# Kernel optimization log

Hardware: AMD Instinct MI355X
Metric: run time of the kernel (lower is better)

The kernel has to match this reference:

```python
import jax, jax.numpy as jnp
import numpy as np

B, S, D = 2, 2048, 512
E, H, TOP_K = 8, 1024, 2
SCALE = 1.0


def setup_inputs() -> dict:
    key = jax.random.key(0)
    ks = jax.random.split(key, 7)
    s = lambda fan_in: 1.0 / np.sqrt(fan_in)
    return {
        "x": jax.random.normal(ks[0], (B, S, D), dtype=jnp.float32),
        "gate_w": jax.random.normal(ks[1], (E, D), dtype=jnp.float32) * s(D),
        "w1": jax.random.normal(ks[2], (E, H, D), dtype=jnp.float32) * s(D),
        "w2": jax.random.normal(ks[3], (E, D, H), dtype=jnp.float32) * s(H),
        "sg_gate": jax.random.normal(ks[4], (H, D), dtype=jnp.float32) * s(D),
        "sg_up": jax.random.normal(ks[5], (H, D), dtype=jnp.float32) * s(D),
        "sg_down": jax.random.normal(ks[6], (D, H), dtype=jnp.float32) * s(H),
    }


def reference(x, gate_w, w1, w2, sg_gate, sg_up, sg_down):
    b, s_len, d = x.shape
    xf = x.reshape(-1, d)                      # [N, D]
    n = xf.shape[0]

    # --- TopKRouter: logits -> top-k -> softmax over the k selected logits ---
    logits = (xf @ gate_w.T) * SCALE           # [N, E]
    topk_w, idx = jax.lax.top_k(logits, TOP_K)  # [N, K]
    topk_w = jax.nn.softmax(topk_w, axis=-1)
    # per-token combine weights scattered to expert slots: [N, E]
    comb = jnp.zeros((n, E), dtype=xf.dtype).at[jnp.arange(n)[:, None], idx].add(topk_w)

    # --- Routed experts (dense masked compute; weight 0 for unrouted) ---
    h = jax.nn.silu(jnp.einsum('td,ehd->teh', xf, w1))   # [N, E, H]
    eo = jnp.einsum('teh,edh->ted', h, w2)               # [N, E, D]
    routed = jnp.einsum('te,ted->td', comb, eo)          # [N, D]

    # --- Shared expert (SwiGLU), n_shared_experts = 1 ---
    shared = (jax.nn.silu(xf @ sg_gate.T) * (xf @ sg_up.T)) @ sg_down.T

    return (routed + shared).reshape(b, s_len, d)
```

## Files before the change

### kernel.cpp

```cpp
#include <hip/hip_runtime.h>
#include <hip/hip_bf16.h>


#define NTOK 4096
#define DDIM 512
#define HDIM 1024
#define NEXP 8
#define CAP  4096

typedef unsigned short u16;
typedef __attribute__((ext_vector_type(8))) short short8;
typedef __attribute__((ext_vector_type(4))) float f32x4;

__device__ __forceinline__ u16 f2bf(float f) {
  unsigned u = __float_as_uint(f);
  u += 0x7fffu + ((u >> 16) & 1u);
  return (u16)(u >> 16);
}
__device__ __forceinline__ float bf2f(u16 v) {
  return __uint_as_float(((unsigned)v) << 16);
}
__device__ __forceinline__ float silu_f(float v) { return v / (1.0f + __expf(-v)); }

__device__ __forceinline__ void gload16(const u16* g, u16* l) {
  __builtin_amdgcn_global_load_lds((const __attribute__((address_space(1))) void*)g,
                                   (__attribute__((address_space(3))) void*)l, 16, 0, 0);
}

__global__ __launch_bounds__(256) void prep(
    const float* __restrict__ x,   const float* __restrict__ gw,
    const float* __restrict__ w1,
    const float* __restrict__ sgg, const float* __restrict__ sgu,
    u16* __restrict__ Xb, u16* __restrict__ W1b,
    u16* __restrict__ SGGb, u16* __restrict__ SGUb,
    int* __restrict__ tIdx, float2* __restrict__ tW) {
  if (blockIdx.x < NTOK / 4) {
    const int lane = threadIdx.x & 63;
    const int wid  = threadIdx.x >> 6;
    const int t = blockIdx.x * 4 + wid;
    const float4* xr = (const float4*)(x + (size_t)t * DDIM + lane * 8);
    const float4 x0 = xr[0], x1 = xr[1];
    short8 xbv;
    xbv[0]=f2bf(x0.x); xbv[1]=f2bf(x0.y); xbv[2]=f2bf(x0.z); xbv[3]=f2bf(x0.w);
    xbv[4]=f2bf(x1.x); xbv[5]=f2bf(x1.y); xbv[6]=f2bf(x1.z); xbv[7]=f2bf(x1.w);
    *(short8*)&Xb[(size_t)t * DDIM + lane * 8] = xbv;
    float p[NEXP];
#pragma unroll
    for (int e = 0; e < NEXP; ++e) {
      const float4* gr = (const float4*)(gw + (size_t)e * DDIM + lane * 8);
      const float4 g0 = gr[0], g1 = gr[1];
      p[e] = x0.x*g0.x + x0.y*g0.y + x0.z*g0.z + x0.w*g0.w +
             x1.x*g1.x + x1.y*g1.y + x1.z*g1.z + x1.w*g1.w;
    }
#pragma unroll
    for (int e = 0; e < NEXP; ++e) {
#pragma unroll
      for (int m = 32; m >= 1; m >>= 1) p[e] += __shfl_xor(p[e], m);
    }
    if (lane == 0) {
      int i0 = 0; float v0 = p[0];
#pragma unroll
      for (int e = 1; e < NEXP; ++e) if (p[e] > v0) { v0 = p[e]; i0 = e; }
      int i1 = -1; float v1 = -3.0e38f;
#pragma unroll
      for (int e = 0; e < NEXP; ++e) if (e != i0 && p[e] > v1) { v1 = p[e]; i1 = e; }
      const float ex1 = __expf(v1 - v0);
      const float inv = 1.0f / (1.0f + ex1);
      tIdx[t] = i0 | (i1 << 4);
      tW[t] = make_float2(inv, ex1 * inv);
    }
  } else {
    constexpr int NW1 = NEXP * HDIM * DDIM / 4;
    constexpr int NSG = HDIM * DDIM / 4;
    constexpr int TOT = NW1 + 2 * NSG;
    int i = (blockIdx.x - NTOK / 4) * 256 + threadIdx.x;
    const int stride = (gridDim.x - NTOK / 4) * 256;
    for (; i < TOT; i += stride) {
      const float* s; u16* d; int j = i;
      if (j < NW1)               { s = w1;  d = W1b;  }
      else if ((j -= NW1) < NSG) { s = sgg; d = SGGb; }
      else        { j -= NSG;      s = sgu; d = SGUb; }
      float4 v = ((const float4*)s)[j];
      ushort4 o;
      o.x = f2bf(v.x); o.y = f2bf(v.y); o.z = f2bf(v.z); o.w = f2bf(v.w);
      ((ushort4*)d)[j] = o;
    }
  }
}

__global__ __launch_bounds__(256) void build_lists(
    const int* __restrict__ tIdx,
    int* __restrict__ counts, int* __restrict__ elist) {
  const int e = blockIdx.x;
  __shared__ int cnt;
  if (threadIdx.x == 0) cnt = 0;
  __syncthreads();
  const int lane = threadIdx.x & 63;
  int* el = elist + e * CAP;
  for (int base = 0; base < NTOK; base += 256) {
    const int t = base + threadIdx.x;
    const int pk = tIdx[t];
#pragma unroll
    for (int slot = 0; slot < 2; ++slot) {
      const bool m = (((pk >> (slot * 4)) & 15) == e);
      const unsigned long long b = __ballot(m);
      const int my  = __popcll(b & ((1ull << lane) - 1));
      const int tot = __popcll(b);
      int wbase = 0;
      if (lane == 0 && tot) wbase = atomicAdd(&cnt, tot);
      wbase = __shfl(wbase, 0);
      if (m) el[wbase + my] = t * 2 + slot;
    }
  }
  __syncthreads();
  if (threadIdx.x == 0) counts[e] = cnt;
}

#define BUFE (128 * 32)

__global__ __launch_bounds__(512, 6) void gemm_up(
    const u16* __restrict__ Xb, const u16* __restrict__ W1b,
    const u16* __restrict__ SGGb, const u16* __restrict__ SGUb,
    const float* __restrict__ w2f, const float* __restrict__ sgdf,
    u16* __restrict__ W2b, u16* __restrict__ SGDb,
    u16* __restrict__ Hbuf, u16* __restrict__ ACT,
    const int* __restrict__ counts, const int* __restrict__ elist) {
  constexpr int KDIM = DDIM, KSTEP = KDIM / 32;
  const int z = blockIdx.z;

  if (z == 0) {
    constexpr int NW2 = NEXP * DDIM * HDIM / 4;
    constexpr int NSG = HDIM * DDIM / 4;
    constexpr int TOT = NW2 + NSG;
    const int cb = blockIdx.x + 16 * blockIdx.y;
    int i = cb * 512 + threadIdx.x;
    const int stride = 512 * 512;
    for (; i < TOT; i += stride) {
      const float* s; u16* d; int j = i;
      if (j < NW2) { s = w2f; d = W2b; }
      else         { j -= NW2; s = sgdf; d = SGDb; }
      float4 v = ((const float4*)s)[j];
      ushort4 o;
      o.x = f2bf(v.x); o.y = f2bf(v.y); o.z = f2bf(v.z); o.w = f2bf(v.w);
      ((ushort4*)d)[j] = o;
    }
    return;
  }

  const int m0 = blockIdx.y * 128;
  const bool routed = (z <= NEXP);

  int mlim; const u16* Bp = nullptr; const int* lst = nullptr;
  if (routed) {
    const int e = z - 1;
    if (blockIdx.x >= 8) return;
    mlim = counts[e];
    lst = elist + e * CAP;
    Bp = W1b + (size_t)e * HDIM * KDIM;
  } else {
    mlim = NTOK;
  }
  if (m0 >= mlim) return;

  __shared__ __align__(16) u16 As[3 * BUFE];
  __shared__ __align__(16) u16 Bs[3 * BUFE];
  __shared__ int rowE[128];

  const int tid = threadIdx.x;
  const int wid = tid >> 6, lane = tid & 63;

  if (routed) {
    if (tid < 128) {
      int idx = m0 + tid; if (idx > mlim - 1) idx = mlim - 1;
      rowE[tid] = lst[idx];
    }
    __syncthreads();
  }

  const int row = tid >> 2;
  const int kcp = ((tid & 3) - ((row >> 1) & 3)) & 3;
  const int arow = routed ? (rowE[row] >> 1) : (m0 + row);
  const u16* aG = Xb + (size_t)arow * KDIM + kcp * 8;
  const u16* bG;
  if (routed) {
    bG = Bp + (size_t)(blockIdx.x * 128 + row) * KDIM + kcp * 8;
  } else {
    const int n0 = blockIdx.x * 64;
    bG = (row < 64) ? SGGb + (size_t)(n0 + row) * KDIM + kcp * 8
                    : SGUb + (size_t)(n0 + row - 64) * KDIM + kcp * 8;
  }

  const int lr = lane & 15, lk = lane >> 4;
  const int rslot = ((lk + ((lr >> 1) & 3)) & 3) * 8;

  auto STAGE = [&](int kt, int c) {
    gload16(aG + kt * 32, As + c * BUFE + tid * 8);
    gload16(bG + kt * 32, Bs + c * BUFE + tid * 8);
  };

  const f32x4 zero = {0.f, 0.f, 0.f, 0.f};

  if (routed) {
    const int n0 = blockIdx.x * 128;
    const int wm = (wid >> 2) * 64, wn = (wid & 3) * 32;
    f32x4 acc[4][2];
#pragma unroll
    for (int i = 0; i < 4; ++i)
#pragma unroll
      for (int j = 0; j < 2; ++j) acc[i][j] = zero;

    STAGE(0, 0); STAGE(1, 1);
    for (int kt = 0; kt < KSTEP; ++kt) {
      if (kt + 1 < KSTEP) asm volatile("s_waitcnt vmcnt(2)" ::: "memory");
      else                asm volatile("s_waitcnt vmcnt(0)" ::: "memory");
      __builtin_amdgcn_s_barrier();
      __builtin_amdgcn_sched_barrier(0);
      if (kt + 2 < KSTEP) STAGE(kt + 2, (kt + 2) % 3);
      const u16* ab = As + (kt % 3) * BUFE;
      const u16* bb = Bs + (kt % 3) * BUFE;
      short8 a[4], b[2];
#pragma unroll
      for (int i = 0; i < 4; ++i)
        a[i] = *(const short8*)&ab[(wm + i * 16 + lr) * 32 + rslot];
#pragma unroll
      for (int j = 0; j < 2; ++j)
        b[j] = *(const short8*)&bb[(wn + j * 16 + lr) * 32 + rslot];
      __builtin_amdgcn_s_setprio(1);
#pragma unroll
      for (int i = 0; i < 4; ++i)
#pragma unroll
        for (int j = 0; j < 2; ++j)
          acc[i][j] = __builtin_amdgcn_mfma_f32_16x16x32_bf16(a[i], b[j], acc[i][j], 0, 0, 0);
      __builtin_amdgcn_s_setprio(0);
    }

#pragma unroll
    for (int i = 0; i < 4; ++i) {
#pragma unroll
      for (int j = 0; j < 2; ++j) {
        const int col = n0 + wn + j * 16 + lr;
#pragma unroll
        for (int r = 0; r < 4; ++r) {
          const int m = wm + i * 16 + lk * 4 + r;
          if (m0 + m < mlim)
            Hbuf[(size_t)rowE[m] * HDIM + col] = f2bf(silu_f(acc[i][j][r]));
        }
      }
    }
  } else {
    const int n0 = blockIdx.x * 64;
    const int wm = (wid >> 2) * 64, ws = (wid & 3) * 16;
    f32x4 ag[4], au[4];
#pragma unroll
    for (int i = 0; i < 4; ++i) { ag[i] = zero; au[i] = zero; }

    STAGE(0, 0); STAGE(1, 1);
    for (int kt = 0; kt < KSTEP; ++kt) {
      if (kt + 1 < KSTEP) asm volatile("s_waitcnt vmcnt(2)" ::: "memory");
      else                asm volatile("s_waitcnt vmcnt(0)" ::: "memory");
      __builtin_amdgcn_s_barrier();
      __builtin_amdgcn_sched_barrier(0);
      if (kt + 2 < KSTEP) STAGE(kt + 2, (kt + 2) % 3);
      const u16* ab = As + (kt % 3) * BUFE;
      const u16* bb = Bs + (kt % 3) * BUFE;
      short8 a[4], bg, bu;
#pragma unroll
      for (int i = 0; i < 4; ++i)
        a[i] = *(const short8*)&ab[(wm + i * 16 + lr) * 32 + rslot];
      bg = *(const short8*)&bb[(ws + lr) * 32 + rslot];
      bu = *(const short8*)&bb[(64 + ws + lr) * 32 + rslot];
      __builtin_amdgcn_s_setprio(1);
#pragma unroll
      for (int i = 0; i < 4; ++i) {
        ag[i] = __builtin_amdgcn_mfma_f32_16x16x32_bf16(a[i], bg, ag[i], 0, 0, 0);
        au[i] = __builtin_amdgcn_mfma_f32_16x16x32_bf16(a[i], bu, au[i], 0, 0, 0);
      }
      __builtin_amdgcn_s_setprio(0);
    }

#pragma unroll
    for (int i = 0; i < 4; ++i) {
      const int col = n0 + ws + lr;
#pragma unroll
      for (int r = 0; r < 4; ++r) {
        const int m = wm + i * 16 + lk * 4 + r;
        ACT[(size_t)(m0 + m) * HDIM + col] = f2bf(silu_f(ag[i][r]) * au[i][r]);
      }
    }
  }
}

__global__ __launch_bounds__(512, 6) void gemm_down(
    const u16* __restrict__ Hbuf, const u16* __restrict__ W2b,
    const u16* __restrict__ ACT,  const u16* __restrict__ SGDb,
    u16* __restrict__ eo0, u16* __restrict__ eo1,
    float* __restrict__ sh0, float* __restrict__ sh1,
    const int* __restrict__ counts, const int* __restrict__ elist) {
  constexpr int KFULL = HDIM;
  constexpr int KSTEP = 512 / 32;
  const int z = blockIdx.z;
  const int n0 = blockIdx.x * 128;
  const int m0 = blockIdx.y * 128;
  const bool routed = (z < 2 * NEXP);
  const int khalf = routed ? (z & 1) : (z - 2 * NEXP);
  const int koff = khalf * 512;

  int mlim; const u16* Ap; const u16* Bp; const int* lst = nullptr;
  if (routed) {
    const int e = z >> 1;
    mlim = counts[e];
    lst = elist + e * CAP;
    Ap = Hbuf;
    Bp = W2b + (size_t)e * DDIM * KFULL;
  } else {
    mlim = NTOK;
    Ap = ACT;
    Bp = SGDb;
  }
  if (m0 >= mlim) return;

  __shared__ __align__(16) u16 As[3 * BUFE];
  __shared__ __align__(16) u16 Bs[3 * BUFE];
  __shared__ int rowE[128];

  const int tid = threadIdx.x;
  const int wid = tid >> 6, lane = tid & 63;

  if (routed) {
    if (tid < 128) {
      int idx = m0 + tid; if (idx > mlim - 1) idx = mlim - 1;
      rowE[tid] = lst[idx];
    }
    __syncthreads();
  }

  const int row = tid >> 2;
  const int kcp = ((tid & 3) - ((row >> 1) & 3)) & 3;
  const int arow = routed ? rowE[row] : (m0 + row);
  const u16* aG = Ap + (size_t)arow * KFULL + koff + kcp * 8;
  const u16* bG = Bp + (size_t)(n0 + row) * KFULL + koff + kcp * 8;

  const int wm = (wid >> 2) * 64, wn = (wid & 3) * 32;
  const int lr = lane & 15, lk = lane >> 4;
  const int rslot = ((lk + ((lr >> 1) & 3)) & 3) * 8;

  const f32x4 zero = {0.f, 0.f, 0.f, 0.f};
  f32x4 acc[4][2];
#pragma unroll
  for (int i = 0; i < 4; ++i)
#pragma unroll
    for (int j = 0; j < 2; ++j) acc[i][j] = zero;

  auto STAGE = [&](int kt, int c) {
    gload16(aG + kt * 32, As + c * BUFE + tid * 8);
    gload16(bG + kt * 32, Bs + c * BUFE + tid * 8);
  };

  STAGE(0, 0); STAGE(1, 1);
  for (int kt = 0; kt < KSTEP; ++kt) {
    if (kt + 1 < KSTEP) asm volatile("s_waitcnt vmcnt(2)" ::: "memory");
    else                asm volatile("s_waitcnt vmcnt(0)" ::: "memory");
    __builtin_amdgcn_s_barrier();
    __builtin_amdgcn_sched_barrier(0);
    if (kt + 2 < KSTEP) STAGE(kt + 2, (kt + 2) % 3);
    const u16* ab = As + (kt % 3) * BUFE;
    const u16* bb = Bs + (kt % 3) * BUFE;
    short8 a[4], b[2];
#pragma unroll
    for (int i = 0; i < 4; ++i)
      a[i] = *(const short8*)&ab[(wm + i * 16 + lr) * 32 + rslot];
#pragma unroll
    for (int j = 0; j < 2; ++j)
      b[j] = *(const short8*)&bb[(wn + j * 16 + lr) * 32 + rslot];
    __builtin_amdgcn_s_setprio(1);
#pragma unroll
    for (int i = 0; i < 4; ++i)
#pragma unroll
      for (int j = 0; j < 2; ++j)
        acc[i][j] = __builtin_amdgcn_mfma_f32_16x16x32_bf16(a[i], b[j], acc[i][j], 0, 0, 0);
    __builtin_amdgcn_s_setprio(0);
  }

#pragma unroll
  for (int i = 0; i < 4; ++i) {
#pragma unroll
    for (int j = 0; j < 2; ++j) {
      const int col = n0 + wn + j * 16 + lr;
#pragma unroll
      for (int r = 0; r < 4; ++r) {
        const int m = wm + i * 16 + lk * 4 + r;
        if (routed) {
          if (m0 + m < mlim) {
            u16* dst = khalf ? eo1 : eo0;
            dst[(size_t)rowE[m] * DDIM + col] = f2bf(acc[i][j][r]);
          }
        } else {
          float* dst = khalf ? sh1 : sh0;
          dst[(size_t)(m0 + m) * DDIM + col] = acc[i][j][r];
        }
      }
    }
  }
}

__global__ __launch_bounds__(256) void combine_kernel(
    const u16* __restrict__ eo0, const u16* __restrict__ eo1,
    const float* __restrict__ sh0, const float* __restrict__ sh1,
    const float2* __restrict__ tW, float* __restrict__ out) {
  const int g = blockIdx.x * 256 + threadIdx.x;
  const int t = g >> 6;
  const int c0 = (g & 63) * 8;
  const float2 w = tW[t];
  const size_t r0 = (size_t)(t * 2) * DDIM + c0;
  const size_t r1 = (size_t)(t * 2 + 1) * DDIM + c0;
  const short8 a0 = *(const short8*)&eo0[r0];
  const short8 a1 = *(const short8*)&eo0[r1];
  const short8 b0 = *(const short8*)&eo1[r0];
  const short8 b1 = *(const short8*)&eo1[r1];
  const size_t so = (size_t)t * DDIM + c0;
  const float4 s0a = ((const float4*)(sh0 + so))[0];
  const float4 s0b = ((const float4*)(sh0 + so))[1];
  const float4 s1a = ((const float4*)(sh1 + so))[0];
  const float4 s1b = ((const float4*)(sh1 + so))[1];
  float o[8];
  o[0]=s0a.x+s1a.x; o[1]=s0a.y+s1a.y; o[2]=s0a.z+s1a.z; o[3]=s0a.w+s1a.w;
  o[4]=s0b.x+s1b.x; o[5]=s0b.y+s1b.y; o[6]=s0b.z+s1b.z; o[7]=s0b.w+s1b.w;
#pragma unroll
  for (int k = 0; k < 8; ++k)
    o[k] += w.x * (bf2f((u16)a0[k]) + bf2f((u16)b0[k])) +
            w.y * (bf2f((u16)a1[k]) + bf2f((u16)b1[k]));
  float4 v0 = {o[0], o[1], o[2], o[3]};
  float4 v1 = {o[4], o[5], o[6], o[7]};
  ((float4*)(out + so))[0] = v0;
  ((float4*)(out + so))[1] = v1;
}

extern "C" void kernel_launch(void* const* d_in, const int* in_sizes, int n_in,
                              void* d_out, int out_size, void* d_ws, size_t ws_size,
                              hipStream_t stream) {
  const float* x    = (const float*)d_in[0];
  const float* gw   = (const float*)d_in[1];
  const float* w1   = (const float*)d_in[2];
  const float* w2   = (const float*)d_in[3];
  const float* sgg  = (const float*)d_in[4];
  const float* sgu  = (const float*)d_in[5];
  const float* sgd  = (const float*)d_in[6];
  float* out = (float*)d_out;

  char* ws = (char*)d_ws;
  size_t off = 0;
  auto take = [&](size_t bytes) {
    size_t r = off; off += (bytes + 255) & ~(size_t)255; return r;
  };
  int*    counts = (int*)   (ws + take(NEXP * sizeof(int)));
  int*    elist  = (int*)   (ws + take((size_t)NEXP * CAP * sizeof(int)));
  int*    tIdx   = (int*)   (ws + take((size_t)NTOK * sizeof(int)));
  float2* tW     = (float2*)(ws + take((size_t)NTOK * sizeof(float2)));
  u16*    Xb     = (u16*)   (ws + take((size_t)NTOK * DDIM * 2));
  u16*    W1b    = (u16*)   (ws + take((size_t)NEXP * HDIM * DDIM * 2));
  u16*    W2b    = (u16*)   (ws + take((size_t)NEXP * DDIM * HDIM * 2));
  u16*    SGGb   = (u16*)   (ws + take((size_t)HDIM * DDIM * 2));
  u16*    SGUb   = (u16*)   (ws + take((size_t)HDIM * DDIM * 2));
  u16*    SGDb   = (u16*)   (ws + take((size_t)DDIM * HDIM * 2));
  u16*    Hbuf   = (u16*)   (ws + take((size_t)NTOK * 2 * HDIM * 2));
  u16*    ACT    = (u16*)   (ws + take((size_t)NTOK * HDIM * 2));
  u16*    eo0    = (u16*)   (ws + take((size_t)NTOK * 2 * DDIM * 2));
  u16*    eo1    = (u16*)   (ws + take((size_t)NTOK * 2 * DDIM * 2));
  float*  sh0    = (float*) (ws + take((size_t)NTOK * DDIM * 4));
  float*  sh1    = (float*) (ws + take((size_t)NTOK * DDIM * 4));
  if (off > ws_size) return;

  prep<<<dim3(3072), 256, 0, stream>>>(x, gw, w1, sgg, sgu,
                                       Xb, W1b, SGGb, SGUb, tIdx, tW);
  build_lists<<<NEXP, 256, 0, stream>>>(tIdx, counts, elist);
  gemm_up<<<dim3(16, 32, NEXP + 2), 512, 0, stream>>>(
      Xb, W1b, SGGb, SGUb, w2, sgd, W2b, SGDb, Hbuf, ACT, counts, elist);
  gemm_down<<<dim3(DDIM / 128, 32, 2 * NEXP + 2), 512, 0, stream>>>(
      Hbuf, W2b, ACT, SGDb, eo0, eo1, sh0, sh1, counts, elist);
  combine_kernel<<<NTOK * 64 / 256, 256, 0, stream>>>(eo0, eo1, sh0, sh1, tW, out);
}
```

Baseline: 105.0 us.

## Widen GEMM output tiles to 128x256 in up and down projections

Doubles the N dimension of each block tile in gemm_up and gemm_down (routed 128x256, shared 128 gate+128 up columns), so each wave computes a 64x64 sub-tile with 16 MFMA accumulators. The goal is more MFMA work per LDS load of the A operand and fewer blocks re-reading the same activation rows. The cost is more shared memory and registers per block, lowered to an occupancy target of 4, and half as many blocks in a grid that is already sparse for the routed experts.

```diff
diff --git a/kernel.cpp b/kernel.cpp
--- a/kernel.cpp
+++ b/kernel.cpp
@@ -116,9 +116,10 @@
   if (threadIdx.x == 0) counts[e] = cnt;
 }
 
-#define BUFE (128 * 32)
-
-__global__ __launch_bounds__(512, 6) void gemm_up(
+#define ABUF (128 * 32)
+#define BBUF (256 * 32)
+
+__global__ __launch_bounds__(512, 4) void gemm_up(
     const u16* __restrict__ Xb, const u16* __restrict__ W1b,
     const u16* __restrict__ SGGb, const u16* __restrict__ SGUb,
     const float* __restrict__ w2f, const float* __restrict__ sgdf,
@@ -132,9 +133,9 @@
     constexpr int NW2 = NEXP * DDIM * HDIM / 4;
     constexpr int NSG = HDIM * DDIM / 4;
     constexpr int TOT = NW2 + NSG;
-    const int cb = blockIdx.x + 16 * blockIdx.y;
+    const int cb = blockIdx.x + 8 * blockIdx.y;
     int i = cb * 512 + threadIdx.x;
-    const int stride = 512 * 512;
+    const int stride = 256 * 512;
     for (; i < TOT; i += stride) {
       const float* s; u16* d; int j = i;
       if (j < NW2) { s = w2f; d = W2b; }
@@ -152,8 +153,8 @@
 
   int mlim; const u16* Bp = nullptr; const int* lst = nullptr;
   if (routed) {
+    if (blockIdx.x >= 4) return;
     const int e = z - 1;
-    if (blockIdx.x >= 8) return;
     mlim = counts[e];
     lst = elist + e * CAP;
     Bp = W1b + (size_t)e * HDIM * KDIM;
@@ -162,8 +163,8 @@
   }
   if (m0 >= mlim) return;
 
-  __shared__ __align__(16) u16 As[3 * BUFE];
-  __shared__ __align__(16) u16 Bs[3 * BUFE];
+  __shared__ __align__(16) u16 As[3 * ABUF];
+  __shared__ __align__(16) u16 Bs[3 * BBUF];
   __shared__ int rowE[128];
 
   const int tid = threadIdx.x;
@@ -177,59 +178,65 @@
     __syncthreads();
   }
 
-  const int row = tid >> 2;
-  const int kcp = ((tid & 3) - ((row >> 1) & 3)) & 3;
-  const int arow = routed ? (rowE[row] >> 1) : (m0 + row);
-  const u16* aG = Xb + (size_t)arow * KDIM + kcp * 8;
-  const u16* bG;
+  const int rowA = tid >> 2;
+  const int rowB0 = rowA, rowB1 = 128 + rowA;
+  const int kcpA  = ((tid & 3) - ((rowA  >> 1) & 3)) & 3;
+  const int kcpB0 = ((tid & 3) - ((rowB0 >> 1) & 3)) & 3;
+  const int kcpB1 = ((tid & 3) - ((rowB1 >> 1) & 3)) & 3;
+  const int arow = routed ? (rowE[rowA] >> 1) : (m0 + rowA);
+  const u16* aG = Xb + (size_t)arow * KDIM + kcpA * 8;
+  const u16 *bG0, *bG1;
   if (routed) {
-    bG = Bp + (size_t)(blockIdx.x * 128 + row) * KDIM + kcp * 8;
+    const int n0 = blockIdx.x * 256;
+    bG0 = Bp + (size_t)(n0 + rowB0) * KDIM + kcpB0 * 8;
+    bG1 = Bp + (size_t)(n0 + rowB1) * KDIM + kcpB1 * 8;
   } else {
-    const int n0 = blockIdx.x * 64;
-    bG = (row < 64) ? SGGb + (size_t)(n0 + row) * KDIM + kcp * 8
-                    : SGUb + (size_t)(n0 + row - 64) * KDIM + kcp * 8;
+    const int n0 = blockIdx.x * 128;
+    bG0 = SGGb + (size_t)(n0 + rowB0) * KDIM + kcpB0 * 8;
+    bG1 = SGUb + (size_t)(n0 + rowB1 - 128) * KDIM + kcpB1 * 8;
   }
 
   const int lr = lane & 15, lk = lane >> 4;
   const int rslot = ((lk + ((lr >> 1) & 3)) & 3) * 8;
 
   auto STAGE = [&](int kt, int c) {
-    gload16(aG + kt * 32, As + c * BUFE + tid * 8);
-    gload16(bG + kt * 32, Bs + c * BUFE + tid * 8);
+    gload16(aG  + kt * 32, As + c * ABUF + tid * 8);
+    gload16(bG0 + kt * 32, Bs + c * BBUF + tid * 8);
+    gload16(bG1 + kt * 32, Bs + c * BBUF + (tid + 512) * 8);
   };
 
   const f32x4 zero = {0.f, 0.f, 0.f, 0.f};
 
   if (routed) {
-    const int n0 = blockIdx.x * 128;
-    const int wm = (wid >> 2) * 64, wn = (wid & 3) * 32;
-    f32x4 acc[4][2];
+    const int n0 = blockIdx.x * 256;
+    const int wm = (wid >> 2) * 64, wn = (wid & 3) * 64;
+    f32x4 acc[4][4];
 #pragma unroll
     for (int i = 0; i < 4; ++i)
 #pragma unroll
-      for (int j = 0; j < 2; ++j) acc[i][j] = zero;
+      for (int j = 0; j < 4; ++j) acc[i][j] = zero;
 
     STAGE(0, 0); STAGE(1, 1);
     for (int kt = 0; kt < KSTEP; ++kt) {
-      if (kt + 1 < KSTEP) asm volatile("s_waitcnt vmcnt(2)" ::: "memory");
+      if (kt + 1 < KSTEP) asm volatile("s_waitcnt vmcnt(3)" ::: "memory");
       else                asm volatile("s_waitcnt vmcnt(0)" ::: "memory");
       __builtin_amdgcn_s_barrier();
       __builtin_amdgcn_sched_barrier(0);
       if (kt + 2 < KSTEP) STAGE(kt + 2, (kt + 2) % 3);
-      const u16* ab = As + (kt % 3) * BUFE;
-      const u16* bb = Bs + (kt % 3) * BUFE;
-      short8 a[4], b[2];
+      const u16* ab = As + (kt % 3) * ABUF;
+      const u16* bb = Bs + (kt % 3) * BBUF;
+      short8 a[4], b[4];
 #pragma unroll
       for (int i = 0; i < 4; ++i)
         a[i] = *(const short8*)&ab[(wm + i * 16 + lr) * 32 + rslot];
 #pragma unroll
-      for (int j = 0; j < 2; ++j)
+      for (int j = 0; j < 4; ++j)
         b[j] = *(const short8*)&bb[(wn + j * 16 + lr) * 32 + rslot];
       __builtin_amdgcn_s_setprio(1);
 #pragma unroll
       for (int i = 0; i < 4; ++i)
 #pragma unroll
-        for (int j = 0; j < 2; ++j)
+        for (int j = 0; j < 4; ++j)
           acc[i][j] = __builtin_amdgcn_mfma_f32_16x16x32_bf16(a[i], b[j], acc[i][j], 0, 0, 0);
       __builtin_amdgcn_s_setprio(0);
     }
@@ -237,7 +244,7 @@
 #pragma unroll
     for (int i = 0; i < 4; ++i) {
 #pragma unroll
-      for (int j = 0; j < 2; ++j) {
+      for (int j = 0; j < 4; ++j) {
         const int col = n0 + wn + j * 16 + lr;
 #pragma unroll
         for (int r = 0; r < 4; ++r) {
@@ -248,49 +255,60 @@
       }
     }
   } else {
-    const int n0 = blockIdx.x * 64;
-    const int wm = (wid >> 2) * 64, ws = (wid & 3) * 16;
-    f32x4 ag[4], au[4];
-#pragma unroll
-    for (int i = 0; i < 4; ++i) { ag[i] = zero; au[i] = zero; }
+    const int n0 = blockIdx.x * 128;
+    const int wm = (wid >> 2) * 64, ws = (wid & 3) * 32;
+    f32x4 ag[4][2], au[4][2];
+#pragma unroll
+    for (int i = 0; i < 4; ++i)
+#pragma unroll
+      for (int j = 0; j < 2; ++j) { ag[i][j] = zero; au[i][j] = zero; }
 
     STAGE(0, 0); STAGE(1, 1);
     for (int kt = 0; kt < KSTEP; ++kt) {
-      if (kt + 1 < KSTEP) asm volatile("s_waitcnt vmcnt(2)" ::: "memory");
+      if (kt + 1 < KSTEP) asm volatile("s_waitcnt vmcnt(3)" ::: "memory");
       else                asm volatile("s_waitcnt vmcnt(0)" ::: "memory");
       __builtin_amdgcn_s_barrier();
       __builtin_amdgcn_sched_barrier(0);
       if (kt + 2 < KSTEP) STAGE(kt + 2, (kt + 2) % 3);
-      const u16* ab = As + (kt % 3) * BUFE;
-      const u16* bb = Bs + (kt % 3) * BUFE;
-      short8 a[4], bg, bu;
+      const u16* ab = As + (kt % 3) * ABUF;
+      const u16* bb = Bs + (kt % 3) * BBUF;
+      short8 a[4], bg[2], bu[2];
 #pragma unroll
       for (int i = 0; i < 4; ++i)
         a[i] = *(const short8*)&ab[(wm + i * 16 + lr) * 32 + rslot];
-      bg = *(const short8*)&bb[(ws + lr) * 32 + rslot];
-      bu = *(const short8*)&bb[(64 + ws + lr) * 32 + rslot];
+#pragma unroll
+      for (int j = 0; j < 2; ++j) {
+        bg[j] = *(const short8*)&bb[(ws + j * 16 + lr) * 32 + rslot];
+        bu[j] = *(const short8*)&bb[(128 + ws + j * 16 + lr) * 32 + rslot];
+      }
       __builtin_amdgcn_s_setprio(1);
 #pragma unroll
-      for (int i = 0; i < 4; ++i) {
-        ag[i] = __builtin_amdgcn_mfma_f32_16x16x32_bf16(a[i], bg, ag[i], 0, 0, 0);
-        au[i] = __builtin_amdgcn_mfma_f32_16x16x32_bf16(a[i], bu, au[i], 0, 0, 0);
+      for (int i = 0; i < 4; ++i)
+#pragma unroll
+        for (int j = 0; j < 2; ++j) {
+          ag[i][j] = __builtin_amdgcn_mfma_f32_16x16x32_bf16(a[i], bg[j], ag[i][j], 0, 0, 0);
+          au[i][j] = __builtin_amdgcn_mfma_f32_16x16x32_bf16(a[i], bu[j], au[i][j], 0, 0, 0);
+        }
+      __builtin_amdgcn_s_setprio(0);
+    }
+
+#pragma unroll
+    for (int i = 0; i < 4; ++i) {
+#pragma unroll
+      for (int j = 0; j < 2; ++j) {
+        const int col = n0 + ws + j * 16 + lr;
+#pragma unroll
+        for (int r = 0; r < 4; ++r) {
+          const int m = wm + i * 16 + lk * 4 + r;
+          ACT[(size_t)(m0 + m) * HDIM + col] =
+              f2bf(silu_f(ag[i][j][r]) * au[i][j][r]);
+        }
       }
-      __builtin_amdgcn_s_setprio(0);
-    }
-
-#pragma unroll
-    for (int i = 0; i < 4; ++i) {
-      const int col = n0 + ws + lr;
-#pragma unroll
-      for (int r = 0; r < 4; ++r) {
-        const int m = wm + i * 16 + lk * 4 + r;
-        ACT[(size_t)(m0 + m) * HDIM + col] = f2bf(silu_f(ag[i][r]) * au[i][r]);
-      }
-    }
-  }
-}
-
-__global__ __launch_bounds__(512, 6) void gemm_down(
+    }
+  }
+}
+
+__global__ __launch_bounds__(512, 4) void gemm_down(
     const u16* __restrict__ Hbuf, const u16* __restrict__ W2b,
     const u16* __restrict__ ACT,  const u16* __restrict__ SGDb,
     u16* __restrict__ eo0, u16* __restrict__ eo1,
@@ -299,7 +317,7 @@
   constexpr int KFULL = HDIM;
   constexpr int KSTEP = 512 / 32;
   const int z = blockIdx.z;
-  const int n0 = blockIdx.x * 128;
+  const int n0 = blockIdx.x * 256;
   const int m0 = blockIdx.y * 128;
   const bool routed = (z < 2 * NEXP);
   const int khalf = routed ? (z & 1) : (z - 2 * NEXP);
@@ -319,8 +337,8 @@
   }
   if (m0 >= mlim) return;
 
-  __shared__ __align__(16) u16 As[3 * BUFE];
-  __shared__ __align__(16) u16 Bs[3 * BUFE];
+  __shared__ __align__(16) u16 As[3 * ABUF];
+  __shared__ __align__(16) u16 Bs[3 * BBUF];
   __shared__ int rowE[128];
 
   const int tid = threadIdx.x;
@@ -334,49 +352,54 @@
     __syncthreads();
   }
 
-  const int row = tid >> 2;
-  const int kcp = ((tid & 3) - ((row >> 1) & 3)) & 3;
-  const int arow = routed ? rowE[row] : (m0 + row);
-  const u16* aG = Ap + (size_t)arow * KFULL + koff + kcp * 8;
-  const u16* bG = Bp + (size_t)(n0 + row) * KFULL + koff + kcp * 8;
-
-  const int wm = (wid >> 2) * 64, wn = (wid & 3) * 32;
+  const int rowA = tid >> 2;
+  const int rowB0 = rowA, rowB1 = 128 + rowA;
+  const int kcpA  = ((tid & 3) - ((rowA  >> 1) & 3)) & 3;
+  const int kcpB0 = ((tid & 3) - ((rowB0 >> 1) & 3)) & 3;
+  const int kcpB1 = ((tid & 3) - ((rowB1 >> 1) & 3)) & 3;
+  const int arow = routed ? rowE[rowA] : (m0 + rowA);
+  const u16* aG  = Ap + (size_t)arow * KFULL + koff + kcpA * 8;
+  const u16* bG0 = Bp + (size_t)(n0 + rowB0) * KFULL + koff + kcpB0 * 8;
+  const u16* bG1 = Bp + (size_t)(n0 + rowB1) * KFULL + koff + kcpB1 * 8;
+
+  const int wm = (wid >> 2) * 64, wn = (wid & 3) * 64;
   const int lr = lane & 15, lk = lane >> 4;
   const int rslot = ((lk + ((lr >> 1) & 3)) & 3) * 8;
 
   const f32x4 zero = {0.f, 0.f, 0.f, 0.f};
-  f32x4 acc[4][2];
+  f32x4 acc[4][4];
 #pragma unroll
   for (int i = 0; i < 4; ++i)
 #pragma unroll
-    for (int j = 0; j < 2; ++j) acc[i][j] = zero;
+    for (int j = 0; j < 4; ++j) acc[i][j] = zero;
 
   auto STAGE = [&](int kt, int c) {
-    gload16(aG + kt * 32, As + c * BUFE + tid * 8);
-    gload16(bG + kt * 32, Bs + c * BUFE + tid * 8);
+    gload16(aG  + kt * 32, As + c * ABUF + tid * 8);
+    gload16(bG0 + kt * 32, Bs + c * BBUF + tid * 8);
+    gload16(bG1 + kt * 32, Bs + c * BBUF + (tid + 512) * 8);
   };
 
   STAGE(0, 0); STAGE(1, 1);
   for (int kt = 0; kt < KSTEP; ++kt) {
-    if (kt + 1 < KSTEP) asm volatile("s_waitcnt vmcnt(2)" ::: "memory");
+    if (kt + 1 < KSTEP) asm volatile("s_waitcnt vmcnt(3)" ::: "memory");
     else                asm volatile("s_waitcnt vmcnt(0)" ::: "memory");
     __builtin_amdgcn_s_barrier();
     __builtin_amdgcn_sched_barrier(0);
     if (kt + 2 < KSTEP) STAGE(kt + 2, (kt + 2) % 3);
-    const u16* ab = As + (kt % 3) * BUFE;
-    const u16* bb = Bs + (kt % 3) * BUFE;
-    short8 a[4], b[2];
+    const u16* ab = As + (kt % 3) * ABUF;
+    const u16* bb = Bs + (kt % 3) * BBUF;
+    short8 a[4], b[4];
 #pragma unroll
     for (int i = 0; i < 4; ++i)
       a[i] = *(const short8*)&ab[(wm + i * 16 + lr) * 32 + rslot];
 #pragma unroll
-    for (int j = 0; j < 2; ++j)
+    for (int j = 0; j < 4; ++j)
       b[j] = *(const short8*)&bb[(wn + j * 16 + lr) * 32 + rslot];
     __builtin_amdgcn_s_setprio(1);
 #pragma unroll
     for (int i = 0; i < 4; ++i)
 #pragma unroll
-      for (int j = 0; j < 2; ++j)
+      for (int j = 0; j < 4; ++j)
         acc[i][j] = __builtin_amdgcn_mfma_f32_16x16x32_bf16(a[i], b[j], acc[i][j], 0, 0, 0);
     __builtin_amdgcn_s_setprio(0);
   }
@@ -384,7 +407,7 @@
 #pragma unroll
   for (int i = 0; i < 4; ++i) {
 #pragma unroll
-    for (int j = 0; j < 2; ++j) {
+    for (int j = 0; j < 4; ++j) {
       const int col = n0 + wn + j * 16 + lr;
 #pragma unroll
       for (int r = 0; r < 4; ++r) {
@@ -473,9 +496,9 @@
   prep<<<dim3(3072), 256, 0, stream>>>(x, gw, w1, sgg, sgu,
                                        Xb, W1b, SGGb, SGUb, tIdx, tW);
   build_lists<<<NEXP, 256, 0, stream>>>(tIdx, counts, elist);
-  gemm_up<<<dim3(16, 32, NEXP + 2), 512, 0, stream>>>(
+  gemm_up<<<dim3(8, 32, NEXP + 2), 512, 0, stream>>>(
       Xb, W1b, SGGb, SGUb, w2, sgd, W2b, SGDb, Hbuf, ACT, counts, elist);
-  gemm_down<<<dim3(DDIM / 128, 32, 2 * NEXP + 2), 512, 0, stream>>>(
+  gemm_down<<<dim3(2, 32, 2 * NEXP + 2), 512, 0, stream>>>(
       Hbuf, W2b, ACT, SGDb, eo0, eo1, sh0, sh1, counts, elist);
   combine_kernel<<<NTOK * 64 / 256, 256, 0, stream>>>(eo0, eo1, sh0, sh1, tW, out);
 }
```

Measured after the change: 112.5 us. 7.1% more time.
